# Kernel tuning notes

Measured on AMD Instinct MI355X. Metric: run time of the kernel, lower is better.

## Reference

```python
import jax, jax.numpy as jnp
import numpy as np

SEQ_LEN = 2048
DIM = 1024
K = 24
N_FFT = 4096  # nearest power of two >= 2*seq_len - 1


def setup_inputs() -> dict:
    key = jax.random.key(0)
    k1, k2, k3, k4 = jax.random.split(key, 4)
    x = jax.random.normal(k1, (4, SEQ_LEN, DIM), dtype=jnp.float32)
    filters = jax.random.normal(k2, (SEQ_LEN, K), dtype=jnp.float32) * 0.1
    M_inputs = jax.random.normal(k3, (DIM, DIM), dtype=jnp.float32) * (DIM ** -0.5)
    M_filters = jax.random.normal(k4, (K, DIM), dtype=jnp.float32) * (K ** -0.5)
    input_pos = jnp.arange(SEQ_LEN, dtype=jnp.int32)
    return {"x": x, "filters": filters, "M_inputs": M_inputs,
            "M_filters": M_filters, "input_pos": input_pos}


def reference(x, filters, M_inputs, M_filters, input_pos):
    # STU forward, use_approx=True, use_hankel_L=False, no flash_fft, no cache.
    B, S, D = x.shape
    # alternating sign +1,-1,+1,... along sequence
    sgn = jnp.where(jnp.arange(S) % 2 == 0, 1.0, -1.0).astype(x.dtype)[None, :, None]
    x_proj = x @ M_inputs                      # (B, S, D)
    phi_proj = filters @ M_filters             # (S, D)
    # v: (1, S, D, 1) -> rfft over seq axis with length N_FFT
    V = jnp.fft.rfft(phi_proj[None, :, :, None], n=N_FFT, axis=1)
    # U: stack [u, u*sgn] on last axis -> (B, S, D, 2)
    U = jnp.fft.rfft(jnp.stack([x_proj, x_proj * sgn], axis=-1), n=N_FFT, axis=1)
    U_conv = jnp.fft.irfft(V * U, n=N_FFT, axis=1)[:, :S]   # (B, S, D, 2)
    spectral_plus = U_conv[..., 0]
    spectral_minus = U_conv[..., 1] * sgn
    return spectral_plus + spectral_minus
```

## Files before the change

### kernel.cpp

```cpp
#include <hip/hip_runtime.h>
#include <hip/hip_bf16.h>
#include <stdint.h>
#include <stddef.h>

#define DIM 1024
#define SEQ 2048
#define KF 24

using f32x4  = __attribute__((ext_vector_type(4))) float;
using bf16x8 = __attribute__((ext_vector_type(8))) short;

__device__ __forceinline__ float bf2f(unsigned short u){
  union { unsigned int i; float f; } v; v.i = ((unsigned int)u) << 16; return v.f;
}
__device__ __forceinline__ unsigned short f2bf(float f){
  union { float f; unsigned int i; } v; v.f = f;
  unsigned int r = v.i + 0x7FFFu + ((v.i >> 16) & 1u);
  return (unsigned short)(r >> 16);
}
__device__ __forceinline__ float dot2bf(unsigned int a, unsigned int b, float c){
  float d;
  asm("v_dot2_f32_bf16 %0, %1, %2, %3" : "=v"(d) : "v"(a), "v"(b), "v"(c));
  return d;
}
__device__ __forceinline__ void gload_lds16(const void* g, void* l){
  __builtin_amdgcn_global_load_lds(
      (const __attribute__((address_space(1))) unsigned int*)g,
      (__attribute__((address_space(3))) unsigned int*)l, 16, 0, 0);
}

__global__ void k_cvt_x(const float* __restrict__ x, unsigned short* __restrict__ xb){
  int i = blockIdx.x * 256 + threadIdx.x;
  const float4* x4 = (const float4*)x;
  float4 v = x4[i];
  ushort4 o;
  o.x = f2bf(v.x); o.y = f2bf(v.y); o.z = f2bf(v.z); o.w = f2bf(v.w);
  *(ushort4*)(xb + (size_t)i * 4) = o;
}

__global__ void k_tr_M(const float* __restrict__ Mi, unsigned short* __restrict__ MbT){
  __shared__ float tile[32][33];
  int e0 = blockIdx.y * 32, d0 = blockIdx.x * 32;
  int tx = threadIdx.x, ty = threadIdx.y;
  #pragma unroll
  for (int r = 0; r < 32; r += 8)
    tile[ty + r][tx] = Mi[(size_t)(e0 + ty + r) * DIM + d0 + tx];
  __syncthreads();
  #pragma unroll
  for (int r = 0; r < 32; r += 8)
    MbT[(size_t)(d0 + ty + r) * DIM + e0 + tx] = f2bf(tile[tx][ty + r]);
}

__global__ void k_pe(const float* __restrict__ filters, const float* __restrict__ Mf,
                     unsigned int* __restrict__ pepk){
  int d  = blockIdx.x * 256 + threadIdx.x;
  int r2 = blockIdx.y;
  float a0 = 0.f, a1 = 0.f;
  #pragma unroll
  for (int k = 0; k < KF; ++k){
    float mf = Mf[(size_t)k * DIM + d];
    a0 += filters[(size_t)(4 * r2)     * KF + k] * mf;
    a1 += filters[(size_t)(4 * r2 + 2) * KF + k] * mf;
  }
  unsigned int lo = f2bf(2.f * a0), hi = f2bf(2.f * a1);
  pepk[(size_t)r2 * DIM + d] = lo | (hi << 16);
}

#define BM 128
#define BN 128
#define BKK 64
__global__ void k_gemm(const unsigned short* __restrict__ A,
                       const unsigned short* __restrict__ Bt,
                       unsigned short* __restrict__ C){
  __shared__ unsigned short As[BM * BKK];
  __shared__ unsigned short Bs[BN * BKK];
  int tid  = threadIdx.x;
  int lane = tid & 63, wave = tid >> 6;
  int wm = wave >> 1, wn = wave & 1;
  int trow0 = blockIdx.x * BM;
  int ncol0 = blockIdx.y * BN;

  f32x4 acc[4][4] = {};

  for (int kt = 0; kt < 1024 / BKK; ++kt){
    __syncthreads();
    #pragma unroll
    for (int g = 0; g < 4; ++g){
      int c  = wave * 4 + g;
      int mr = c * 8 + (lane >> 3);
      int u  = lane & 7;
      int su = u ^ (mr & 7);
      const unsigned short* srcA = A + (size_t)(trow0 + mr) * 1024 + kt * BKK + su * 8;
      gload_lds16(srcA, (char*)As + c * 1024);
      const unsigned short* srcB = Bt + (size_t)(ncol0 + mr) * 1024 + kt * BKK + su * 8;
      gload_lds16(srcB, (char*)Bs + c * 1024);
    }
    __syncthreads();

    bf16x8 af[4][2], bfr[4][2];
    #pragma unroll
    for (int mi = 0; mi < 4; ++mi){
      int row = wm * 64 + mi * 16 + (lane & 15);
      #pragma unroll
      for (int ks = 0; ks < 2; ++ks){
        int u = ((lane >> 4) + 4 * ks) ^ (row & 7);
        af[mi][ks] = *(const bf16x8*)((const char*)As + row * 128 + u * 16);
      }
    }
    #pragma unroll
    for (int ni = 0; ni < 4; ++ni){
      int row = wn * 64 + ni * 16 + (lane & 15);
      #pragma unroll
      for (int ks = 0; ks < 2; ++ks){
        int u = ((lane >> 4) + 4 * ks) ^ (row & 7);
        bfr[ni][ks] = *(const bf16x8*)((const char*)Bs + row * 128 + u * 16);
      }
    }
    #pragma unroll
    for (int mi = 0; mi < 4; ++mi)
      #pragma unroll
      for (int ni = 0; ni < 4; ++ni)
        #pragma unroll
        for (int ks = 0; ks < 2; ++ks)
          acc[mi][ni] = __builtin_amdgcn_mfma_f32_16x16x32_bf16(
              af[mi][ks], bfr[ni][ks], acc[mi][ni], 0, 0, 0);
  }

  #pragma unroll
  for (int mi = 0; mi < 4; ++mi)
    #pragma unroll
    for (int ni = 0; ni < 4; ++ni){
      int col = ncol0 + wn * 64 + ni * 16 + (lane & 15);
      #pragma unroll
      for (int reg = 0; reg < 4; ++reg){
        int row = trow0 + wm * 64 + mi * 16 + (lane >> 4) * 4 + reg;
        C[(size_t)row * 1024 + col] = f2bf(acc[mi][ni][reg]);
      }
    }
}

#define MV 16
__device__ __forceinline__ void conv_tile16(const unsigned short* __restrict__ ycol,
                                            const unsigned int* __restrict__ pcol,
                                            float* __restrict__ ocol, int m0){
  float acc[MV];
  #pragma unroll
  for (int m = 0; m < MV; ++m) acc[m] = 0.f;

  unsigned int W[30];
  #pragma unroll
  for (int t = 0; t < 14; ++t) W[t] = 0u;
  {
    unsigned int y0 = ycol[0];
    W[14] = y0;
    unsigned int prev = y0;
    #pragma unroll
    for (int t = 1; t < 16; ++t){
      unsigned int yt = ycol[(size_t)t * 2048];
      W[14 + t] = yt | (prev << 16);
      prev = yt;
    }
  }
  unsigned int prev15 = ycol[(size_t)15 * 2048];

  unsigned int pv[8];
  #pragma unroll
  for (int q = 0; q < 8; ++q) pv[q] = pcol[(size_t)((m0 >> 1) + q) * 1024];

  int nch = (m0 >> 4) + 1;
  for (int c = 0; c + 1 < nch; ++c){
    int j0 = 16 * c;
    int r0 = m0 - 16 * c;
    unsigned int ny[16], npv[8];
    #pragma unroll
    for (int t = 0; t < 16; ++t) ny[t] = ycol[(size_t)(j0 + 16 + t) * 2048];
    #pragma unroll
    for (int q = 0; q < 8; ++q) npv[q] = pcol[(size_t)(((r0 - 16) >> 1) + q) * 1024];

    #pragma unroll
    for (int q = 0; q < 8; ++q)
      #pragma unroll
      for (int m = 0; m < MV; ++m)
        acc[m] = dot2bf(pv[q], W[m + 14 - 2 * q], acc[m]);

    #pragma unroll
    for (int t = 0; t < 14; ++t) W[t] = W[t + 16];
    W[14] = ny[0] | (prev15 << 16);
    #pragma unroll
    for (int t = 1; t < 16; ++t) W[14 + t] = ny[t] | (ny[t - 1] << 16);
    prev15 = ny[15];
    #pragma unroll
    for (int q = 0; q < 8; ++q) pv[q] = npv[q];
  }
  #pragma unroll
  for (int q = 0; q < 8; ++q)
    #pragma unroll
    for (int m = 0; m < MV; ++m)
      acc[m] = dot2bf(pv[q], W[m + 14 - 2 * q], acc[m]);

  #pragma unroll
  for (int m = 0; m < MV; ++m)
    ocol[(size_t)(m0 + m) * 2048] = acc[m];
}

__global__ __launch_bounds__(256, 4)
void k_conv(const unsigned short* __restrict__ xp,
            const unsigned int* __restrict__ pepk,
            float* __restrict__ out){
  int d    = blockIdx.x * 256 + threadIdx.x;
  int pair = blockIdx.y;
  int bp   = blockIdx.z;
  int b = bp >> 1, p = bp & 1;
  const unsigned short* ycol = xp + (size_t)(b * SEQ + p) * DIM + d;
  const unsigned int*   pcol = pepk + d;
  float* ocol = out + (size_t)(b * SEQ + p) * DIM + d;

  conv_tile16(ycol, pcol, ocol, pair * MV);
  conv_tile16(ycol, pcol, ocol, (63 - pair) * MV);
}

extern "C" void kernel_launch(void* const* d_in, const int* in_sizes, int n_in,
                              void* d_out, int out_size, void* d_ws, size_t ws_size,
                              hipStream_t stream){
  const float* x       = (const float*)d_in[0];
  const float* filters = (const float*)d_in[1];
  const float* Mi      = (const float*)d_in[2];
  const float* Mf      = (const float*)d_in[3];

  char* ws = (char*)d_ws;
  unsigned short* Xb   = (unsigned short*)(ws);
  unsigned short* XPb  = (unsigned short*)(ws + (size_t)16 * 1024 * 1024);
  unsigned short* MbT  = (unsigned short*)(ws + (size_t)32 * 1024 * 1024);
  unsigned int*   pepk = (unsigned int*)  (ws + (size_t)34 * 1024 * 1024);
  float* out = (float*)d_out;

  hipLaunchKernelGGL(k_cvt_x, dim3(8192), dim3(256), 0, stream, x, Xb);
  hipLaunchKernelGGL(k_tr_M,  dim3(32, 32), dim3(32, 8), 0, stream, Mi, MbT);
  hipLaunchKernelGGL(k_pe,    dim3(4, 512), dim3(256), 0, stream, filters, Mf, pepk);
  hipLaunchKernelGGL(k_gemm,  dim3(64, 8), dim3(256), 0, stream, Xb, MbT, XPb);
  hipLaunchKernelGGL(k_conv,  dim3(4, 32, 8), dim3(256), 0, stream, XPb, pepk, out);
}
```

Before: 149.8 us.

## Emit pre-paired bf16 words from GEMM and transpose filter spectrum for vector loads

The GEMM epilogue now writes each output element into a 32-bit paired buffer (y[t] in the low half, and as the high half of t+2's word), so the convolution loads ready-made dot2 operands and no longer shifts and ORs neighbours. The filter projection is stored transposed per channel, so the conv kernel fetches 8 packed coefficients with two uint4 loads instead of 8 strided scalar loads. The conv grid changes from paired triangular tiles per block to one tile per block, with blocks ordered longest-first. In exchange the GEMM does twice as many scattered 16-bit stores and the intermediate buffer doubles in size, which adds memory traffic.

New measurement: 189.6 us. 1.27x slower.

```diff
diff --git a/kernel.cpp b/kernel.cpp
--- a/kernel.cpp
+++ b/kernel.cpp
@@ -10,9 +10,6 @@
 using f32x4  = __attribute__((ext_vector_type(4))) float;
 using bf16x8 = __attribute__((ext_vector_type(8))) short;
 
-__device__ __forceinline__ float bf2f(unsigned short u){
-  union { unsigned int i; float f; } v; v.i = ((unsigned int)u) << 16; return v.f;
-}
 __device__ __forceinline__ unsigned short f2bf(float f){
   union { float f; unsigned int i; } v; v.f = f;
   unsigned int r = v.i + 0x7FFFu + ((v.i >> 16) & 1u);
@@ -52,9 +49,9 @@
 }
 
 __global__ void k_pe(const float* __restrict__ filters, const float* __restrict__ Mf,
-                     unsigned int* __restrict__ pepk){
-  int d  = blockIdx.x * 256 + threadIdx.x;
-  int r2 = blockIdx.y;
+                     unsigned int* __restrict__ pepkT){
+  int r2 = blockIdx.x * 256 + threadIdx.x;
+  int d  = blockIdx.y;
   float a0 = 0.f, a1 = 0.f;
   #pragma unroll
   for (int k = 0; k < KF; ++k){
@@ -63,7 +60,7 @@
     a1 += filters[(size_t)(4 * r2 + 2) * KF + k] * mf;
   }
   unsigned int lo = f2bf(2.f * a0), hi = f2bf(2.f * a1);
-  pepk[(size_t)r2 * DIM + d] = lo | (hi << 16);
+  pepkT[(size_t)d * 512 + r2] = lo | (hi << 16);
 }
 
 #define BM 128
@@ -71,7 +68,7 @@
 #define BKK 64
 __global__ void k_gemm(const unsigned short* __restrict__ A,
                        const unsigned short* __restrict__ Bt,
-                       unsigned short* __restrict__ C){
+                       unsigned int* __restrict__ Bg){
   __shared__ unsigned short As[BM * BKK];
   __shared__ unsigned short Bs[BN * BKK];
   int tid  = threadIdx.x;
@@ -126,6 +123,7 @@
               af[mi][ks], bfr[ni][ks], acc[mi][ni], 0, 0, 0);
   }
 
+  unsigned short* Bh = (unsigned short*)Bg;
   #pragma unroll
   for (int mi = 0; mi < 4; ++mi)
     #pragma unroll
@@ -134,15 +132,41 @@
       #pragma unroll
       for (int reg = 0; reg < 4; ++reg){
         int row = trow0 + wm * 64 + mi * 16 + (lane >> 4) * 4 + reg;
-        C[(size_t)row * 1024 + col] = f2bf(acc[mi][ni][reg]);
+        unsigned short y = f2bf(acc[mi][ni][reg]);
+        int t = row & 2047;
+        size_t idx = (size_t)row * 1024 + col;
+        if (t < 2) Bg[idx] = (unsigned int)y;
+        else       Bh[2 * idx] = y;
+        if (t < 2046)
+          Bh[2 * ((size_t)(row + 2) * 1024 + col) + 1] = y;
       }
     }
 }
 
 #define MV 16
-__device__ __forceinline__ void conv_tile16(const unsigned short* __restrict__ ycol,
-                                            const unsigned int* __restrict__ pcol,
-                                            float* __restrict__ ocol, int m0){
+__device__ __forceinline__ void dot_block(uint4 a, uint4 b,
+                                          const unsigned int* __restrict__ W,
+                                          float* __restrict__ acc){
+  const unsigned int pq[8] = {a.x, a.y, a.z, a.w, b.x, b.y, b.z, b.w};
+  #pragma unroll
+  for (int q = 0; q < 8; ++q)
+    #pragma unroll
+    for (int m = 0; m < MV; ++m)
+      acc[m] = dot2bf(pq[q], W[m + 14 - 2 * q], acc[m]);
+}
+
+__global__ __launch_bounds__(256, 4)
+void k_conv(const unsigned int* __restrict__ Bg,
+            const unsigned int* __restrict__ pepkT,
+            float* __restrict__ out){
+  int d  = blockIdx.x * 256 + threadIdx.x;
+  int mt = 63 - blockIdx.y;
+  int bp = blockIdx.z;
+  int b = bp >> 1, p = bp & 1;
+  const unsigned int* bcol = Bg + ((size_t)(b * SEQ + p) * 1024 + d);
+  const unsigned int* pcol = pepkT + (size_t)d * 512;
+  int m0 = mt * MV;
+
   float acc[MV];
   #pragma unroll
   for (int m = 0; m < MV; ++m) acc[m] = 0.f;
@@ -150,73 +174,34 @@
   unsigned int W[30];
   #pragma unroll
   for (int t = 0; t < 14; ++t) W[t] = 0u;
-  {
-    unsigned int y0 = ycol[0];
-    W[14] = y0;
-    unsigned int prev = y0;
-    #pragma unroll
-    for (int t = 1; t < 16; ++t){
-      unsigned int yt = ycol[(size_t)t * 2048];
-      W[14 + t] = yt | (prev << 16);
-      prev = yt;
-    }
+  #pragma unroll
+  for (int t = 0; t < 16; ++t) W[14 + t] = bcol[(size_t)t * 2048];
+
+  uint4 pva = *(const uint4*)(pcol + (m0 >> 1));
+  uint4 pvb = *(const uint4*)(pcol + (m0 >> 1) + 4);
+
+  for (int c = 0; c < mt; ++c){
+    unsigned int nW[16];
+    #pragma unroll
+    for (int t = 0; t < 16; ++t) nW[t] = bcol[(size_t)(16 * c + 16 + t) * 2048];
+    int nr2 = (m0 >> 1) - 8 * (c + 1);
+    uint4 npa = *(const uint4*)(pcol + nr2);
+    uint4 npb = *(const uint4*)(pcol + nr2 + 4);
+
+    dot_block(pva, pvb, W, acc);
+
+    #pragma unroll
+    for (int t = 0; t < 14; ++t) W[t] = W[t + 16];
+    #pragma unroll
+    for (int t = 0; t < 16; ++t) W[14 + t] = nW[t];
+    pva = npa; pvb = npb;
   }
-  unsigned int prev15 = ycol[(size_t)15 * 2048];
-
-  unsigned int pv[8];
-  #pragma unroll
-  for (int q = 0; q < 8; ++q) pv[q] = pcol[(size_t)((m0 >> 1) + q) * 1024];
-
-  int nch = (m0 >> 4) + 1;
-  for (int c = 0; c + 1 < nch; ++c){
-    int j0 = 16 * c;
-    int r0 = m0 - 16 * c;
-    unsigned int ny[16], npv[8];
-    #pragma unroll
-    for (int t = 0; t < 16; ++t) ny[t] = ycol[(size_t)(j0 + 16 + t) * 2048];
-    #pragma unroll
-    for (int q = 0; q < 8; ++q) npv[q] = pcol[(size_t)(((r0 - 16) >> 1) + q) * 1024];
-
-    #pragma unroll
-    for (int q = 0; q < 8; ++q)
-      #pragma unroll
-      for (int m = 0; m < MV; ++m)
-        acc[m] = dot2bf(pv[q], W[m + 14 - 2 * q], acc[m]);
-
-    #pragma unroll
-    for (int t = 0; t < 14; ++t) W[t] = W[t + 16];
-    W[14] = ny[0] | (prev15 << 16);
-    #pragma unroll
-    for (int t = 1; t < 16; ++t) W[14 + t] = ny[t] | (ny[t - 1] << 16);
-    prev15 = ny[15];
-    #pragma unroll
-    for (int q = 0; q < 8; ++q) pv[q] = npv[q];
-  }
-  #pragma unroll
-  for (int q = 0; q < 8; ++q)
-    #pragma unroll
-    for (int m = 0; m < MV; ++m)
-      acc[m] = dot2bf(pv[q], W[m + 14 - 2 * q], acc[m]);
-
+  dot_block(pva, pvb, W, acc);
+
+  float* ocol = out + ((size_t)(b * SEQ + p) * 1024 + d);
   #pragma unroll
   for (int m = 0; m < MV; ++m)
     ocol[(size_t)(m0 + m) * 2048] = acc[m];
-}
-
-__global__ __launch_bounds__(256, 4)
-void k_conv(const unsigned short* __restrict__ xp,
-            const unsigned int* __restrict__ pepk,
-            float* __restrict__ out){
-  int d    = blockIdx.x * 256 + threadIdx.x;
-  int pair = blockIdx.y;
-  int bp   = blockIdx.z;
-  int b = bp >> 1, p = bp & 1;
-  const unsigned short* ycol = xp + (size_t)(b * SEQ + p) * DIM + d;
-  const unsigned int*   pcol = pepk + d;
-  float* ocol = out + (size_t)(b * SEQ + p) * DIM + d;
-
-  conv_tile16(ycol, pcol, ocol, pair * MV);
-  conv_tile16(ycol, pcol, ocol, (63 - pair) * MV);
 }
 
 extern "C" void kernel_launch(void* const* d_in, const int* in_sizes, int n_in,
@@ -228,15 +213,15 @@
   const float* Mf      = (const float*)d_in[3];
 
   char* ws = (char*)d_ws;
-  unsigned short* Xb   = (unsigned short*)(ws);
-  unsigned short* XPb  = (unsigned short*)(ws + (size_t)16 * 1024 * 1024);
-  unsigned short* MbT  = (unsigned short*)(ws + (size_t)32 * 1024 * 1024);
-  unsigned int*   pepk = (unsigned int*)  (ws + (size_t)34 * 1024 * 1024);
+  unsigned short* Xb    = (unsigned short*)(ws);
+  unsigned int*   Bg    = (unsigned int*)  (ws + (size_t)16 * 1024 * 1024);
+  unsigned short* MbT   = (unsigned short*)(ws + (size_t)48 * 1024 * 1024);
+  unsigned int*   pepkT = (unsigned int*)  (ws + (size_t)50 * 1024 * 1024);
   float* out = (float*)d_out;
 
   hipLaunchKernelGGL(k_cvt_x, dim3(8192), dim3(256), 0, stream, x, Xb);
   hipLaunchKernelGGL(k_tr_M,  dim3(32, 32), dim3(32, 8), 0, stream, Mi, MbT);
-  hipLaunchKernelGGL(k_pe,    dim3(4, 512), dim3(256), 0, stream, filters, Mf, pepk);
-  hipLaunchKernelGGL(k_gemm,  dim3(64, 8), dim3(256), 0, stream, Xb, MbT, XPb);
-  hipLaunchKernelGGL(k_conv,  dim3(4, 32, 8), dim3(256), 0, stream, XPb, pepk, out);
-}
+  hipLaunchKernelGGL(k_pe,    dim3(2, 1024), dim3(256), 0, stream, filters, Mf, pepkT);
+  hipLaunchKernelGGL(k_gemm,  dim3(64, 8), dim3(256), 0, stream, Xb, MbT, Bg);
+  hipLaunchKernelGGL(k_conv,  dim3(4, 64, 8), dim3(256), 0, stream, Bg, pepkT, out);
+}
```
